# Kernel optimization log

Hardware: AMD Instinct MI355X
Metric: run time of the kernel (lower is better)

## Reference

```python
import jax, jax.numpy as jnp
import numpy as np

N = 100000
E = 640000
IN_DIM = 128
HID = 128
NUM_REL = 8


def _rgcn_layer(x, rel_w, root_w, bias, src, dst, edge_type, num_nodes):
    # PyG RGCNConv: out = x @ root + bias + sum_r mean_{edges of rel r into v}(x_src) @ W_r
    out = x @ root_w + bias
    x_src = x[src]  # [E, d_in]
    for r in range(NUM_REL):
        w = (edge_type == r).astype(x.dtype)  # [E]
        msg_sum = jax.ops.segment_sum(x_src * w[:, None], dst, num_segments=num_nodes)
        cnt = jax.ops.segment_sum(w, dst, num_segments=num_nodes)
        agg = msg_sum / jnp.maximum(cnt, 1.0)[:, None]  # mean aggregation per relation
        out = out + agg @ rel_w[r]
    return out


def setup_inputs() -> dict:
    key = jax.random.key(0)
    ks = jax.random.split(key, 10)
    x = jax.random.normal(ks[0], (N, IN_DIM), dtype=jnp.float32)
    edge_index = jax.random.randint(ks[1], (2, E), 0, N, dtype=jnp.int64)
    edge_type = jax.random.randint(ks[2], (E,), 0, NUM_REL, dtype=jnp.int64)
    s1 = 1.0 / np.sqrt(IN_DIM)
    s2 = 1.0 / np.sqrt(HID)
    rel_w1 = jax.random.uniform(ks[3], (NUM_REL, IN_DIM, HID), jnp.float32, -s1, s1)
    root_w1 = jax.random.uniform(ks[4], (IN_DIM, HID), jnp.float32, -s1, s1)
    b1 = jnp.zeros((HID,), jnp.float32)
    rel_w2 = jax.random.uniform(ks[5], (NUM_REL, HID, HID), jnp.float32, -s2, s2)
    root_w2 = jax.random.uniform(ks[6], (HID, HID), jnp.float32, -s2, s2)
    b2 = jnp.zeros((HID,), jnp.float32)
    return {"x": x, "edge_index": edge_index, "edge_type": edge_type,
            "rel_w1": rel_w1, "root_w1": root_w1, "b1": b1,
            "rel_w2": rel_w2, "root_w2": root_w2, "b2": b2}


def reference(x, edge_index, edge_type, rel_w1, root_w1, b1, rel_w2, root_w2, b2):
    src, dst = edge_index[0], edge_index[1]
    h = _rgcn_layer(x, rel_w1, root_w1, b1, src, dst, edge_type, N)
    h = jax.nn.relu(h)  # dropout p=0.0 -> identity
    h = _rgcn_layer(h, rel_w2, root_w2, b2, src, dst, edge_type, N)
    h = jax.nn.relu(h)
    return h
```

## Files before the change

kernel.cpp:

```cpp
#include <hip/hip_runtime.h>
#include <hip/hip_bf16.h>

#define NN 100000
#define EE 640000
#define DD 128
#define RR 8
#define K8 (NN * RR)
#define NSB2 196
#define NB 1563
#define AGB 20000

typedef __attribute__((ext_vector_type(8))) short short8;
typedef __attribute__((ext_vector_type(4))) float floatx4;
typedef __attribute__((ext_vector_type(4))) unsigned int uint4v;

__device__ __forceinline__ unsigned short f2bf(float f) {
  unsigned int u = __float_as_uint(f);
  u += 0x7FFFu + ((u >> 16) & 1u);
  return (unsigned short)(u >> 16);
}
__device__ __forceinline__ unsigned int pk2bf(float a, float b) {
  __hip_bfloat162 h = __float22bfloat162_rn(make_float2(a, b));
  unsigned int u;
  __builtin_memcpy(&u, &h, 4);
  return u;
}
__device__ __forceinline__ float bflo(unsigned int u) { return __uint_as_float(u << 16); }
__device__ __forceinline__ float bfhi(unsigned int u) { return __uint_as_float(u & 0xFFFF0000u); }

__global__ __launch_bounds__(256) void xb_prep(
    const float* __restrict__ x, unsigned int* __restrict__ xb)
{
  int g = blockIdx.x * 256 + threadIdx.x;
  int v = g >> 4, seg = g & 15;
  const float4* s4 = (const float4*)(x + (size_t)v * 128 + seg * 8);
  float4 a = s4[0], b = s4[1];
  uint4v o;
  o[0] = pk2bf(a.x, a.y); o[1] = pk2bf(a.z, a.w);
  o[2] = pk2bf(b.x, b.y); o[3] = pk2bf(b.z, b.w);
  *(uint4v*)(xb + (size_t)v * 64 + seg * 4) = o;
}

__global__ __launch_bounds__(256) void w_prep_all(
    const float* __restrict__ rel1, const float* __restrict__ root1,
    const float* __restrict__ rel2, const float* __restrict__ root2,
    unsigned short* __restrict__ wt)
{
  int id = blockIdx.x * 256 + threadIdx.x;
  int set = id >= 147456;
  int rem = id - set * 147456;
  int r = rem >> 14, n = (rem >> 7) & 127, k = rem & 127;
  int kk = k;
  if (set) {
    int u = k >> 1, w2 = u >> 4, m2 = u & 15;
    kk = w2 * 32 + m2 + ((k & 1) << 4);
  }
  const float* rel = set ? rel2 : rel1;
  const float* root = set ? root2 : root1;
  float v = (r < RR) ? rel[((size_t)r * DD + kk) * DD + n] : root[(size_t)kk * DD + n];
  wt[id] = f2bf(v);
}

__global__ __launch_bounds__(256) void count_all(
    const int* __restrict__ ei, const int* __restrict__ et,
    int* __restrict__ cnt, int* __restrict__ erank)
{
  int e = blockIdx.x * 256 + threadIdx.x;
  int dst = ei[EE + e], r = et[e];
  erank[e] = atomicAdd(&cnt[r * NN + dst], 1);
}

__global__ __launch_bounds__(256) void scan_a(
    const int4* __restrict__ c4, int n4, int mode, int* __restrict__ bsum)
{
  int t = threadIdx.x;
  int s = 0;
#pragma unroll
  for (int i = 0; i < 4; ++i) {
    int idx = blockIdx.x * 1024 + i * 256 + t;
    if (idx < n4) {
      int4 v = c4[idx];
      if (mode) s += (v.x > 0) + (v.y > 0) + (v.z > 0) + (v.w > 0);
      else      s += v.x + v.y + v.z + v.w;
    }
  }
  __shared__ int wsum[4];
  for (int d = 32; d; d >>= 1) s += __shfl_xor(s, d, 64);
  if ((t & 63) == 0) wsum[t >> 6] = s;
  __syncthreads();
  if (t == 0) bsum[blockIdx.x] = wsum[0] + wsum[1] + wsum[2] + wsum[3];
}

__global__ void scan_b(const int* __restrict__ bsum, int nsb,
                       int* __restrict__ bbase, int* __restrict__ tot)
{
  int lane = threadIdx.x;
  int v[4]; int s = 0;
#pragma unroll
  for (int i = 0; i < 4; ++i) {
    int idx = lane * 4 + i;
    v[i] = (idx < nsb) ? bsum[idx] : 0; s += v[i];
  }
  int inc = s;
  for (int d = 1; d < 64; d <<= 1) {
    int o = __shfl_up(inc, d, 64);
    if (lane >= d) inc += o;
  }
  int running = inc - s;
#pragma unroll
  for (int i = 0; i < 4; ++i) {
    int idx = lane * 4 + i;
    if (idx < nsb) { bbase[idx] = running; running += v[i]; }
  }
  if (lane == 63 && tot != nullptr) tot[0] = inc;
}

__global__ __launch_bounds__(256) void scan_c(
    const int* __restrict__ cnt, const int* __restrict__ bbase, int n, int mode,
    int* __restrict__ out0)
{
  int t = threadIdx.x;
  int base = blockIdx.x * 4096 + t * 16;
  int v[16]; int s = 0;
#pragma unroll
  for (int i = 0; i < 16; ++i) {
    int idx = base + i;
    v[i] = (idx < n) ? cnt[idx] : 0;
    s += mode ? (v[i] > 0) : v[i];
  }
  int lane = t & 63, wid = t >> 6;
  int inc = s;
  for (int d = 1; d < 64; d <<= 1) {
    int o = __shfl_up(inc, d, 64);
    if (lane >= d) inc += o;
  }
  __shared__ int wsum[4];
  if (lane == 63) wsum[wid] = inc;
  __syncthreads();
  int wb = 0;
  for (int w = 0; w < wid; ++w) wb += wsum[w];
  int running = bbase[blockIdx.x] + wb + (inc - s);
#pragma unroll
  for (int i = 0; i < 16; ++i) {
    int idx = base + i;
    if (idx < n) {
      if (mode) { out0[idx] = (v[i] > 0) ? running : -1; running += (v[i] > 0); }
      else      { out0[idx] = running; running += v[i]; }
    }
  }
  if (!mode && blockIdx.x == 0 && t == 0) out0[n] = EE;
}

__global__ __launch_bounds__(256) void erow_fill(
    const int* __restrict__ pidx, const int* __restrict__ rowptr,
    const int* __restrict__ tot, int* __restrict__ erowptr)
{
  int k = blockIdx.x * 256 + threadIdx.x;
  int p = pidx[k];
  if (p >= 0) erowptr[p] = rowptr[k];
  if (k == 0) erowptr[tot[0]] = EE;
}

__global__ __launch_bounds__(256) void place(
    const int* __restrict__ ei, const int* __restrict__ et,
    const int* __restrict__ rowptr, const int* __restrict__ erank,
    int* __restrict__ recs)
{
  int e = blockIdx.x * 256 + threadIdx.x;
  int src = ei[e], dst = ei[EE + e], r = et[e];
  recs[rowptr[r * NN + dst] + erank[e]] = src;
}

__global__ __launch_bounds__(256) void agg_kernel(
    const unsigned int* __restrict__ Xin,
    const int* __restrict__ erowptr,
    const int* __restrict__ recs,
    unsigned int* __restrict__ Agg)
{
  int gid = blockIdx.x * 256 + threadIdx.x;
  int row = gid >> 3, li = gid & 7;
  int beg = erowptr[row], end = erowptr[row + 1];
  if (end <= beg) return;
  const uint4v* X4 = (const uint4v*)Xin;
  uint4v o0, o1;
  int cnt = end - beg;
  if (cnt == 1) {
    int src = recs[beg];
    const uint4v* xp = X4 + (size_t)src * 16 + li * 2;
    o0 = xp[0]; o1 = xp[1];
  } else {
    float f[16];
#pragma unroll
    for (int j = 0; j < 16; ++j) f[j] = 0.f;
    for (int e = beg; e < end; ++e) {
      int src = recs[e];
      const uint4v* xp = X4 + (size_t)src * 16 + li * 2;
      uint4v u0 = xp[0], u1 = xp[1];
      unsigned um[8];
      *(uint4v*)&um[0] = u0; *(uint4v*)&um[4] = u1;
#pragma unroll
      for (int m = 0; m < 8; ++m) {
        f[2 * m]     += bflo(um[m]);
        f[2 * m + 1] += bfhi(um[m]);
      }
    }
    float sc = 1.0f / (float)cnt;
#pragma unroll
    for (int m = 0; m < 4; ++m) o0[m] = pk2bf(f[2 * m] * sc, f[2 * m + 1] * sc);
#pragma unroll
    for (int m = 0; m < 4; ++m) o1[m] = pk2bf(f[8 + 2 * m] * sc, f[9 + 2 * m] * sc);
  }
  uint4v* op = (uint4v*)Agg + (size_t)row * 16 + li * 2;
  op[0] = o0; op[1] = o1;
}

__global__ __launch_bounds__(256, 4) void gemm_final(
    const unsigned int* __restrict__ Xin,
    const unsigned int* __restrict__ Agg,
    const unsigned short* __restrict__ Wt,
    const int* __restrict__ pidx,
    const float* __restrict__ bias,
    void* __restrict__ outp, int out_bf16)
{
  const int v0 = blockIdx.x * 64;
  __shared__ __align__(16) unsigned short As[64 * 128];
  __shared__ int Pr[8 * 64];

  const int tid = threadIdx.x;
  const int wave = tid >> 6, lane = tid & 63;
  const int quad = lane >> 4, mr = lane & 15;
  const int row = tid >> 2, q = tid & 3;
  const uint4v* Agg4 = (const uint4v*)Agg;
  const uint4v* Xin4 = (const uint4v*)Xin;

  for (int id = tid; id < 512; id += 256) {
    int r = id >> 6, d = id & 63;
    int v = v0 + d;
    Pr[id] = (v < NN) ? pidx[r * NN + v] : -1;
  }

  floatx4 acc[4][2];
#pragma unroll
  for (int mi = 0; mi < 4; ++mi) {
    acc[mi][0] = (floatx4){0.f, 0.f, 0.f, 0.f};
    acc[mi][1] = (floatx4){0.f, 0.f, 0.f, 0.f};
  }
  __syncthreads();

#pragma unroll 1
  for (int r = 0; r < 9; ++r) {
    const unsigned short* wr =
        Wt + (size_t)r * 16384 + (size_t)(wave * 32 + mr) * 128 + quad * 8;
    short8 b0[4], b1[4];
#pragma unroll
    for (int ks = 0; ks < 4; ++ks) {
      b0[ks] = *(const short8*)(wr + ks * 32);
      b1[ks] = *(const short8*)(wr + 16 * 128 + ks * 32);
    }
    const uint4v* sp = nullptr;
    if (r < 8) {
      int p = Pr[r * 64 + row];
      if (p >= 0) sp = Agg4 + (size_t)p * 16 + q * 4;
    } else {
      int v = v0 + row;
      if (v < NN) sp = Xin4 + (size_t)v * 16 + q * 4;
    }
    uint4v vals[4];
#pragma unroll
    for (int c = 0; c < 4; ++c)
      vals[c] = sp ? sp[c] : (uint4v){0u, 0u, 0u, 0u};
#pragma unroll
    for (int c = 0; c < 4; ++c) {
      int pos = (q * 32 + c * 8 + (row & 15) * 8) & 127;
      *(uint4v*)&As[row * 128 + pos] = vals[c];
    }
    __syncthreads();
#pragma unroll
    for (int ks = 0; ks < 4; ++ks) {
      short8 a[4];
#pragma unroll
      for (int mi = 0; mi < 4; ++mi)
        a[mi] = *(const short8*)&As[(mi * 16 + mr) * 128 +
                                    ((ks * 32 + quad * 8 + mr * 8) & 127)];
#pragma unroll
      for (int mi = 0; mi < 4; ++mi) {
        acc[mi][0] = __builtin_amdgcn_mfma_f32_16x16x32_bf16(a[mi], b0[ks], acc[mi][0], 0, 0, 0);
        acc[mi][1] = __builtin_amdgcn_mfma_f32_16x16x32_bf16(a[mi], b1[ks], acc[mi][1], 0, 0, 0);
      }
    }
    __syncthreads();
  }

  float bia0 = bias[wave * 32 + mr], bia1 = bias[wave * 32 + 16 + mr];
#pragma unroll
  for (int mi = 0; mi < 4; ++mi)
#pragma unroll
    for (int rg = 0; rg < 4; ++rg) {
      int rw = mi * 16 + quad * 4 + rg;
      int v = v0 + rw;
      if (v < NN) {
        float c0 = fmaxf(acc[mi][0][rg] + bia0, 0.f);
        float c1 = fmaxf(acc[mi][1][rg] + bia1, 0.f);
        if (out_bf16) {
          ((unsigned int*)outp)[(size_t)v * 64 + wave * 16 + mr] = pk2bf(c0, c1);
        } else {
          float* o = (float*)outp;
          o[(size_t)v * 128 + wave * 32 + mr] = c0;
          o[(size_t)v * 128 + wave * 32 + 16 + mr] = c1;
        }
      }
    }
}

extern "C" void kernel_launch(void* const* d_in, const int* in_sizes, int n_in,
                              void* d_out, int out_size, void* d_ws, size_t ws_size,
                              hipStream_t stream) {
  const float* x       = (const float*)d_in[0];
  const int*   ei      = (const int*)d_in[1];
  const int*   et      = (const int*)d_in[2];
  const float* rel_w1  = (const float*)d_in[3];
  const float* root_w1 = (const float*)d_in[4];
  const float* b1      = (const float*)d_in[5];
  const float* rel_w2  = (const float*)d_in[6];
  const float* root_w2 = (const float*)d_in[7];
  const float* b2      = (const float*)d_in[8];

  char* ws = (char*)d_ws;
  size_t off = 0;
  auto alloc = [&](size_t bytes) { char* p = ws + off; off = (off + bytes + 255) & ~(size_t)255; return p; };
  unsigned int*   Xb    = (unsigned int*)alloc((size_t)NN * 64 * 4);
  unsigned int*   h1    = (unsigned int*)alloc((size_t)NN * 64 * 4);
  unsigned int*   Agg   = (unsigned int*)alloc((size_t)EE * 64 * 4);
  unsigned short* Wt    = (unsigned short*)alloc((size_t)2 * 9 * DD * DD * 2);
  int*            cnt   = (int*)alloc((size_t)K8 * 4);
  int*            erowptr = (int*)alloc((size_t)(EE + 2) * 4);
  char*           zend  = ws + off;
  int*            rowptr= (int*)alloc((size_t)(K8 + 1) * 4);
  int*            pidx  = (int*)alloc((size_t)K8 * 4);
  int*            erank = (int*)alloc((size_t)EE * 4);
  int*            recs  = (int*)alloc((size_t)EE * 4);
  int*            bsumA = (int*)alloc((size_t)NSB2 * 4);
  int*            bbaseA= (int*)alloc((size_t)NSB2 * 4);
  int*            bsumB = (int*)alloc((size_t)NSB2 * 4);
  int*            bbaseB= (int*)alloc((size_t)NSB2 * 4);
  int*            Ptot  = (int*)alloc(64);

  hipMemsetAsync(cnt, 0, (size_t)(zend - (char*)cnt), stream);

  xb_prep<<<(NN * 16) / 256, 256, 0, stream>>>(x, Xb);
  w_prep_all<<<(2 * 9 * DD * DD) / 256, 256, 0, stream>>>(rel_w1, root_w1, rel_w2, root_w2, Wt);
  count_all<<<EE / 256, 256, 0, stream>>>(ei, et, cnt, erank);

  scan_a<<<NSB2, 256, 0, stream>>>((const int4*)cnt, K8 / 4, 0, bsumA);
  scan_b<<<1, 64, 0, stream>>>(bsumA, NSB2, bbaseA, nullptr);
  scan_c<<<NSB2, 256, 0, stream>>>(cnt, bbaseA, K8, 0, rowptr);

  scan_a<<<NSB2, 256, 0, stream>>>((const int4*)cnt, K8 / 4, 1, bsumB);
  scan_b<<<1, 64, 0, stream>>>(bsumB, NSB2, bbaseB, Ptot);
  scan_c<<<NSB2, 256, 0, stream>>>(cnt, bbaseB, K8, 1, pidx);

  erow_fill<<<K8 / 256, 256, 0, stream>>>(pidx, rowptr, Ptot, erowptr);
  place<<<EE / 256, 256, 0, stream>>>(ei, et, rowptr, erank, recs);

  agg_kernel<<<AGB, 256, 0, stream>>>(Xb, erowptr, recs, Agg);
  gemm_final<<<NB, 256, 0, stream>>>(Xb, Agg, Wt, pidx, b1, h1, 1);
  agg_kernel<<<AGB, 256, 0, stream>>>(h1, erowptr, recs, Agg);
  gemm_final<<<NB, 256, 0, stream>>>(h1, Agg, Wt + (size_t)9 * DD * DD, pidx, b2, d_out, 0);
}
```

Before: 439.8 us.

## Double-buffer gemm_final A tiles via direct global-to-LDS loads and prefetch weights

The GEMM's A-operand tile is now loaded with global_load_lds straight into a double-buffered shared-memory array, using a rotated layout that matches the existing swizzled read pattern. The next relation's tile and B fragments are prefetched while the current one runs its MFMAs. Missing rows point at a zeroed workspace row, which removes the per-thread null checks. This hides gather latency and drops register staging, at the cost of twice the LDS, more registers for the prefetched B, and a dependence on the direct-to-LDS address mapping being correct.

```diff
diff --git a/kernel.cpp b/kernel.cpp
--- a/kernel.cpp
+++ b/kernel.cpp
@@ -219,25 +219,59 @@
     const unsigned int* __restrict__ Agg,
     const unsigned short* __restrict__ Wt,
     const int* __restrict__ pidx,
+    const unsigned int* __restrict__ Zrow,
     const float* __restrict__ bias,
     void* __restrict__ outp, int out_bf16)
 {
   const int v0 = blockIdx.x * 64;
-  __shared__ __align__(16) unsigned short As[64 * 128];
+  __shared__ __align__(16) unsigned int As[2][64 * 64];
   __shared__ int Pr[8 * 64];
 
   const int tid = threadIdx.x;
   const int wave = tid >> 6, lane = tid & 63;
   const int quad = lane >> 4, mr = lane & 15;
-  const int row = tid >> 2, q = tid & 3;
-  const uint4v* Agg4 = (const uint4v*)Agg;
-  const uint4v* Xin4 = (const uint4v*)Xin;
+  const int lr0 = lane >> 4;
+  const int j = lane & 15;
 
   for (int id = tid; id < 512; id += 256) {
     int r = id >> 6, d = id & 63;
     int v = v0 + d;
     Pr[id] = (v < NN) ? pidx[r * NN + v] : -1;
   }
+  __syncthreads();
+
+  auto ISSUE = [&](int r, int buf) {
+#pragma unroll
+    for (int i = 0; i < 4; ++i) {
+      int d = wave * 16 + i * 4 + lr0;
+      int rot = i * 4 + lr0;
+      int s = (j - rot) & 15;
+      const unsigned int* base;
+      if (r < 8) {
+        int p = Pr[r * 64 + d];
+        base = (p >= 0) ? (Agg + (size_t)p * 64) : Zrow;
+      } else {
+        int v = v0 + d;
+        base = (v < NN) ? (Xin + (size_t)v * 64) : Zrow;
+      }
+      __builtin_amdgcn_global_load_lds(
+          (const __attribute__((address_space(1))) unsigned int*)(base + s * 4),
+          (__attribute__((address_space(3))) unsigned int*)
+              &As[buf][(wave * 16 + i * 4) * 64],
+          16, 0, 0);
+    }
+  };
+
+  short8 bc0[4], bc1[4], bn0[4], bn1[4];
+  auto LOADB = [&](int r, short8* d0, short8* d1) {
+    const unsigned short* wr =
+        Wt + (size_t)r * 16384 + (size_t)(wave * 32 + mr) * 128 + quad * 8;
+#pragma unroll
+    for (int ks = 0; ks < 4; ++ks) {
+      d0[ks] = *(const short8*)(wr + ks * 32);
+      d1[ks] = *(const short8*)(wr + 16 * 128 + ks * 32);
+    }
+  };
 
   floatx4 acc[4][2];
 #pragma unroll
@@ -245,50 +279,34 @@
     acc[mi][0] = (floatx4){0.f, 0.f, 0.f, 0.f};
     acc[mi][1] = (floatx4){0.f, 0.f, 0.f, 0.f};
   }
+
+  ISSUE(0, 0);
+  LOADB(0, bc0, bc1);
   __syncthreads();
 
 #pragma unroll 1
   for (int r = 0; r < 9; ++r) {
-    const unsigned short* wr =
-        Wt + (size_t)r * 16384 + (size_t)(wave * 32 + mr) * 128 + quad * 8;
-    short8 b0[4], b1[4];
-#pragma unroll
-    for (int ks = 0; ks < 4; ++ks) {
-      b0[ks] = *(const short8*)(wr + ks * 32);
-      b1[ks] = *(const short8*)(wr + 16 * 128 + ks * 32);
-    }
-    const uint4v* sp = nullptr;
     if (r < 8) {
-      int p = Pr[r * 64 + row];
-      if (p >= 0) sp = Agg4 + (size_t)p * 16 + q * 4;
-    } else {
-      int v = v0 + row;
-      if (v < NN) sp = Xin4 + (size_t)v * 16 + q * 4;
-    }
-    uint4v vals[4];
-#pragma unroll
-    for (int c = 0; c < 4; ++c)
-      vals[c] = sp ? sp[c] : (uint4v){0u, 0u, 0u, 0u};
-#pragma unroll
-    for (int c = 0; c < 4; ++c) {
-      int pos = (q * 32 + c * 8 + (row & 15) * 8) & 127;
-      *(uint4v*)&As[row * 128 + pos] = vals[c];
-    }
-    __syncthreads();
+      ISSUE(r + 1, (r + 1) & 1);
+      LOADB(r + 1, bn0, bn1);
+    }
+    const unsigned short* asb = (const unsigned short*)As[r & 1];
 #pragma unroll
     for (int ks = 0; ks < 4; ++ks) {
       short8 a[4];
 #pragma unroll
       for (int mi = 0; mi < 4; ++mi)
-        a[mi] = *(const short8*)&As[(mi * 16 + mr) * 128 +
-                                    ((ks * 32 + quad * 8 + mr * 8) & 127)];
+        a[mi] = *(const short8*)&asb[(mi * 16 + mr) * 128 +
+                                     ((ks * 32 + quad * 8 + mr * 8) & 127)];
 #pragma unroll
       for (int mi = 0; mi < 4; ++mi) {
-        acc[mi][0] = __builtin_amdgcn_mfma_f32_16x16x32_bf16(a[mi], b0[ks], acc[mi][0], 0, 0, 0);
-        acc[mi][1] = __builtin_amdgcn_mfma_f32_16x16x32_bf16(a[mi], b1[ks], acc[mi][1], 0, 0, 0);
+        acc[mi][0] = __builtin_amdgcn_mfma_f32_16x16x32_bf16(a[mi], bc0[ks], acc[mi][0], 0, 0, 0);
+        acc[mi][1] = __builtin_amdgcn_mfma_f32_16x16x32_bf16(a[mi], bc1[ks], acc[mi][1], 0, 0, 0);
       }
     }
     __syncthreads();
+#pragma unroll
+    for (int ks = 0; ks < 4; ++ks) { bc0[ks] = bn0[ks]; bc1[ks] = bn1[ks]; }
   }
 
   float bia0 = bias[wave * 32 + mr], bia1 = bias[wave * 32 + 16 + mr];
@@ -334,6 +352,7 @@
   unsigned short* Wt    = (unsigned short*)alloc((size_t)2 * 9 * DD * DD * 2);
   int*            cnt   = (int*)alloc((size_t)K8 * 4);
   int*            erowptr = (int*)alloc((size_t)(EE + 2) * 4);
+  unsigned int*   Zrow  = (unsigned int*)alloc(256);
   char*           zend  = ws + off;
   int*            rowptr= (int*)alloc((size_t)(K8 + 1) * 4);
   int*            pidx  = (int*)alloc((size_t)K8 * 4);
@@ -363,7 +382,7 @@
   place<<<EE / 256, 256, 0, stream>>>(ei, et, rowptr, erank, recs);
 
   agg_kernel<<<AGB, 256, 0, stream>>>(Xb, erowptr, recs, Agg);
-  gemm_final<<<NB, 256, 0, stream>>>(Xb, Agg, Wt, pidx, b1, h1, 1);
+  gemm_final<<<NB, 256, 0, stream>>>(Xb, Agg, Wt, pidx, Zrow, b1, h1, 1);
   agg_kernel<<<AGB, 256, 0, stream>>>(h1, erowptr, recs, Agg);
-  gemm_final<<<NB, 256, 0, stream>>>(h1, Agg, Wt + (size_t)9 * DD * DD, pidx, b2, d_out, 0);
-}
+  gemm_final<<<NB, 256, 0, stream>>>(h1, Agg, Wt + (size_t)9 * DD * DD, pidx, Zrow, b2, d_out, 0);
+}
```

Result: no change. 437.3 us (-0.6%).
